# Kernel optimization log

Measured on AMD Instinct MI355X. Metric: run time of the kernel, lower is better.

Reference implementation:

```python
import jax, jax.numpy as jnp
import numpy as np

# ---- static config (mirrors YOLOH_Expand cfg) ----
H, W = 200, 200            # feature map size
A = 9                      # num_anchors
C = 80                     # num_classes
M = H * W * A              # total anchors
K = 1000                   # topk NMS candidates
STRIDE = 16
CTR_CLAMP = 32.0
CONF_THRESH = 0.05
NMS_THRESH = 0.6
SCALE_CLAMP = float(np.log(1000.0 / 16))  # DEFAULT_SCALE_CLAMP
ANCHOR_SIZES = np.array([[32,32],[64,64],[128,128],[32,64],[64,32],
                         [64,128],[128,64],[128,256],[256,128]], dtype=np.float32)


def make_anchors():
    # generate_anchors: meshgrid (+0.5)*stride centers, tiled anchor sizes -> (M,4) cxcywh
    ys, xs = np.meshgrid(np.arange(H), np.arange(W), indexing='ij')
    xy = (np.stack([xs, ys], -1).reshape(-1, 2).astype(np.float32) + 0.5) * STRIDE  # (HW,2)
    xy = np.repeat(xy[:, None, :], A, axis=1)                                       # (HW,A,2)
    wh = np.broadcast_to(ANCHOR_SIZES[None], (H * W, A, 2)).astype(np.float32)
    return jnp.asarray(np.concatenate([xy, wh], -1).reshape(-1, 4))


def setup_inputs() -> dict:
    key = jax.random.key(0)
    k1, k2 = jax.random.split(key)
    return {
        'cls_pred': jax.random.normal(k1, (1, M, C), jnp.float32) - 2.0,  # logits, mostly low conf
        'reg_pred': jax.random.normal(k2, (1, M, 4), jnp.float32) * 0.5,
        'anchor_boxes': make_anchors(),
    }


def decode_boxes(anchors, reg):
    # decode_boxes: clamped center offset + clamped log-scale wh -> x1y1x2y2
    ctr_off = jnp.clip(reg[..., :2] * anchors[..., 2:], -CTR_CLAMP, CTR_CLAMP)
    ctr_xy = anchors[..., :2] + ctr_off
    dwdh = jnp.minimum(reg[..., 2:], SCALE_CLAMP)
    wh = anchors[..., 2:] * jnp.exp(dwdh)
    return jnp.concatenate([ctr_xy - 0.5 * wh, ctr_xy + 0.5 * wh], axis=-1)


def pairwise_iou(b):
    # exact math of YOLOH_Expand.nms
    x1, y1, x2, y2 = b[:, 0], b[:, 1], b[:, 2], b[:, 3]
    areas = (x2 - x1) * (y2 - y1)
    xx1 = jnp.maximum(x1[:, None], x1[None, :])
    yy1 = jnp.maximum(y1[:, None], y1[None, :])
    xx2 = jnp.minimum(x2[:, None], x2[None, :])
    yy2 = jnp.minimum(y2[:, None], y2[None, :])
    w = jnp.maximum(1e-28, xx2 - xx1)
    h = jnp.maximum(1e-28, yy2 - yy1)
    inter = w * h
    return inter / (areas[:, None] + areas[None, :] - inter + 1e-14)


def greedy_nms_keep(iou, cls_ids, valid):
    # per-class greedy NMS over score-sorted candidates: box i is suppressed if
    # any kept higher-score box j of the same class has IoU > thresh.
    same = cls_ids[:, None] == cls_ids[None, :]           # (K,K)
    idx = jnp.arange(K)

    def body(keep, i):
        prior = idx < i
        sup = jnp.any(keep & prior & same[i] & (iou[i] > NMS_THRESH))
        keep = keep.at[i].set((~sup) & valid[i])
        return keep, None

    keep0 = jnp.zeros((K,), dtype=bool)
    keep, _ = jax.lax.scan(body, keep0, idx)
    return keep


def reference(cls_pred, reg_pred, anchor_boxes):
    scores = jax.nn.sigmoid(cls_pred[0])                  # (M,C)
    boxes = decode_boxes(anchor_boxes, reg_pred[0])       # (M,4)
    # postprocess: per-anchor best class + confidence threshold
    cls_inds = jnp.argmax(scores, axis=1)                 # (M,)
    sc = jnp.max(scores, axis=1)                          # (M,)
    valid = sc >= CONF_THRESH
    # fixed-size top-k candidate set (invalid ranked last)
    _, top_i = jax.lax.top_k(jnp.where(valid, sc, -1.0), K)
    b = boxes[top_i]                                      # (K,4)
    s = sc[top_i]                                         # (K,)
    c = cls_inds[top_i]                                   # (K,)
    v = valid[top_i]                                      # (K,)
    iou = pairwise_iou(b)                                 # (K,K)
    keep = greedy_nms_keep(iou, c, v)                     # (K,) bool
    return b, s * keep.astype(s.dtype), c.astype(jnp.int32), keep
```

## Files before the change

kernel.cpp:

```cpp
#include <hip/hip_runtime.h>
#include <math.h>

typedef unsigned long long u64;
typedef unsigned int u32;

#define M_ANCH 360000
#define NCLS 80
#define KTOP 1000
#define CAP 8192
#define NBINS 65536
#define RREP 8
#define CONF_THRESH 0.05f
#define NMS_THRESH 0.6f
#define CTR_CLAMP 32.0f
#define SCALE_CLAMP 4.1351665567423560f

#define AS1 __attribute__((address_space(1)))
#define AS3 __attribute__((address_space(3)))

#define HIST_OFF   0u
#define HIST_BYTES (RREP * NBINS * 4u)
#define CNT_OFF    (HIST_OFF + HIST_BYTES)
#define B_OFF      (CNT_OFF + 4u)
#define VW_OFF     (B_OFF + 4u + 8u)
#define ZERO_END   (VW_OFF + 128u)
#define MERGED_OFF ZERO_END
#define BLKSUM_OFF (MERGED_OFF + NBINS * 4u)
#define CAND_OFF   (BLKSUM_OFF + 256u)
#define SC_OFF     (CAND_OFF + CAP * 8u)
#define CLS_OFF    (SC_OFF + M_ANCH * 4u)
#define SSC_OFF    (CLS_OFF + M_ANCH * 4u)
#define SCLS_OFF   (SSC_OFF + KTOP * 4u)
#define SUP_OFF    ((SCLS_OFF + KTOP * 4u + 15u) & ~15u)

__device__ __forceinline__ u32 fkey(float f) {
    u32 u = __float_as_uint(f);
    return (u & 0x80000000u) ? ~u : (u | 0x80000000u);
}

__global__ __launch_bounds__(256) void k_score(const float* __restrict__ cls_pred,
                                               float* __restrict__ sc_all,
                                               int* __restrict__ cls_all,
                                               u32* __restrict__ hist) {
    __shared__ float4 stage[1280];
    int t = threadIdx.x;
    const float4* gp = (const float4*)cls_pred + (size_t)blockIdx.x * 1280;
#pragma unroll
    for (int k = 0; k < 5; k++) {
        int f = t + 256 * k;
        __builtin_amdgcn_global_load_lds((AS1 void*)(gp + f),
                                         (AS3 void*)(stage + f), 16, 0, 0);
    }
    __syncthreads();

    if (t < 64) {
        const float4* av = stage + t * 20;
        float mv = -1e30f; int mc = 0;
        int k0 = t & 7;
#pragma unroll
        for (int i = 0; i < 20; i++) {
            int k = k0 + i;
            if (k >= 20) k -= 20;
            float4 v = av[k];
            float lm_ = v.x; int lc_ = 4 * k;
            if (v.y > lm_) { lm_ = v.y; lc_ = 4 * k + 1; }
            if (v.z > lm_) { lm_ = v.z; lc_ = 4 * k + 2; }
            if (v.w > lm_) { lm_ = v.w; lc_ = 4 * k + 3; }
            if (lm_ > mv || (lm_ == mv && lc_ < mc)) { mv = lm_; mc = lc_; }
        }
        int a = blockIdx.x * 64 + t;
        float sc = 1.0f / (1.0f + expf(-mv));
        sc_all[a] = sc;
        cls_all[a] = mc;
        float msk = (sc >= CONF_THRESH) ? sc : -1.0f;
        u32 u = fkey(msk);
        atomicAdd(&hist[((blockIdx.x & (RREP - 1)) << 16) + (u >> 16)], 1u);
    }
}

__global__ __launch_bounds__(1024) void k_hsum(const u32* __restrict__ hist,
                                               u32* __restrict__ merged,
                                               u32* __restrict__ blksum) {
    __shared__ u32 red[1024];
    int t = threadIdx.x;
    int b = blockIdx.x * 1024 + t;
    u32 s = 0;
#pragma unroll
    for (int r = 0; r < RREP; r++) s += hist[r * NBINS + b];
    merged[b] = s;
    red[t] = s;
    __syncthreads();
    for (int off = 512; off > 0; off >>= 1) {
        if (t < off) red[t] += red[t + off];
        __syncthreads();
    }
    if (t == 0) blksum[blockIdx.x] = red[0];
}

__global__ __launch_bounds__(1024) void k_boundary(const u32* __restrict__ merged,
                                                   const u32* __restrict__ blksum,
                                                   u32* __restrict__ outB) {
    __shared__ u32 bs[64];
    __shared__ u32 sj, sA;
    __shared__ u32 csum[1024];
    int t = threadIdx.x;
    if (t < 64) bs[t] = blksum[t];
    __syncthreads();
    if (t == 0) {
        u32 cum = 0; u32 j = 0; u32 Aj = 0;
        for (int b = 63; b >= 0; b--) {
            if (cum + bs[b] >= KTOP) { j = (u32)b; Aj = cum; break; }
            cum += bs[b];
        }
        sj = j; sA = Aj;
    }
    __syncthreads();
    u32 j = sj, Aj = sA;
    u32 h = merged[j * 1024 + t];
    csum[t] = h;
    __syncthreads();
    u32 v = h;
    for (int off = 1; off < 1024; off <<= 1) {
        u32 add = (t + off < 1024) ? csum[t + off] : 0u;
        __syncthreads();
        v += add;
        csum[t] = v;
        __syncthreads();
    }
    u32 above = (t == 1023) ? 0u : csum[t + 1];
    if (Aj + above < KTOP && Aj + above + h >= KTOP) outB[0] = j * 1024 + t;
}

__global__ __launch_bounds__(256) void k_compact(const float* __restrict__ sc_all,
                                                 const u32* __restrict__ pB,
                                                 u32* __restrict__ counter,
                                                 u64* __restrict__ cand) {
    int i = blockIdx.x * 256 + threadIdx.x;
    if (i >= M_ANCH) return;
    u32 B = *pB;
    float s = sc_all[i];
    float m = (s >= CONF_THRESH) ? s : -1.0f;
    u32 u = fkey(m);
    if ((u >> 16) >= B) {
        u32 pos = atomicAdd(counter, 1u);
        if (pos < CAP) cand[pos] = ((u64)u << 32) | (u64)(0xFFFFFFFFu - (u32)i);
    }
}

__global__ __launch_bounds__(1024) void k_select(const u64* __restrict__ cand,
                                                 const u32* __restrict__ counter,
                                                 const float* __restrict__ sc_all,
                                                 const int* __restrict__ cls_all,
                                                 const float* __restrict__ reg_pred,
                                                 const float* __restrict__ anchors,
                                                 float* __restrict__ out,
                                                 float* __restrict__ sel_sc,
                                                 int* __restrict__ sel_cls,
                                                 u64* __restrict__ valid_words) {
    __shared__ u64 keys[CAP];
    int t = threadIdx.x;
    u32 n = *counter;
    if (n > CAP) n = CAP;
    u32 P = 1024;
    while (P < n) P <<= 1;
    for (u32 i = t; i < P; i += 1024) keys[i] = (i < n) ? cand[i] : 0ull;
    for (u32 k = 2; k <= P; k <<= 1) {
        for (u32 j = k >> 1; j > 0; j >>= 1) {
            __syncthreads();
            for (u32 i = t; i < P; i += 1024) {
                u32 ixj = i ^ j;
                if (ixj > i) {
                    u64 a = keys[i], b = keys[ixj];
                    bool desc = ((i & k) == 0);
                    if (desc ? (a < b) : (a > b)) { keys[i] = b; keys[ixj] = a; }
                }
            }
        }
    }
    __syncthreads();
    if (t < KTOP) {
        u64 key = keys[t];
        u32 idx = 0xFFFFFFFFu - (u32)(key & 0xFFFFFFFFull);
        if (idx >= M_ANCH) idx = 0;
        float s = sc_all[idx];
        int cl = cls_all[idx];
        float4 a = ((const float4*)anchors)[idx];
        float4 r = ((const float4*)reg_pred)[idx];
        float ox = fminf(fmaxf(r.x * a.z, -CTR_CLAMP), CTR_CLAMP);
        float oy = fminf(fmaxf(r.y * a.w, -CTR_CLAMP), CTR_CLAMP);
        float cx = a.x + ox, cy = a.y + oy;
        float ww = a.z * expf(fminf(r.z, SCALE_CLAMP));
        float hh = a.w * expf(fminf(r.w, SCALE_CLAMP));
        float4 box;
        box.x = cx - 0.5f * ww;
        box.y = cy - 0.5f * hh;
        box.z = cx + 0.5f * ww;
        box.w = cy + 0.5f * hh;
        ((float4*)out)[t] = box;
        out[5 * KTOP + t] = (float)cl;
        sel_sc[t] = s;
        sel_cls[t] = cl;
        if (s >= CONF_THRESH) atomicOr(&valid_words[t >> 6], 1ull << (t & 63));
    }
}

__global__ __launch_bounds__(256) void k_supmat(const float* __restrict__ out,
                                                const int* __restrict__ sel_cls,
                                                u64* __restrict__ sup) {
    int wid = threadIdx.x >> 6;
    int lane = threadIdx.x & 63;
    int g = blockIdx.x * 4 + wid;
    int i = g >> 4;
    int w = g & 15;
    int j = w * 64 + lane;
    int jc = (j < KTOP) ? j : (KTOP - 1);
    float4 bi = ((const float4*)out)[i];
    float4 bj = ((const float4*)out)[jc];
    int ci = sel_cls[i], cj = sel_cls[jc];
    float ai = (bi.z - bi.x) * (bi.w - bi.y);
    float aj = (bj.z - bj.x) * (bj.w - bj.y);
    float xx1 = fmaxf(bi.x, bj.x), yy1 = fmaxf(bi.y, bj.y);
    float xx2 = fminf(bi.z, bj.z), yy2 = fminf(bi.w, bj.w);
    float iw = fmaxf(1e-28f, xx2 - xx1), ih = fmaxf(1e-28f, yy2 - yy1);
    float inter = iw * ih;
    float iou = inter / (ai + aj - inter + 1e-14f);
    bool pred = (j < i) && (ci == cj) && (iou > NMS_THRESH);
    u64 bal = __ballot((int)pred);
    if (lane == 0) sup[g] = bal;
}

__global__ __launch_bounds__(64) void k_nms(const u64* __restrict__ sup,
                                            const u64* __restrict__ valid_words,
                                            const float* __restrict__ sel_sc,
                                            float* __restrict__ out) {
    __shared__ u64 keepA[16];
    int lane = threadIdx.x;
    if (lane < 16) keepA[lane] = 0ull;
    __syncthreads();

    for (int b = 0; b < 16; b++) {
        int row = b * 64 + lane;
        int rowc = (row < KTOP) ? row : (KTOP - 1);
        const ulonglong2* rp = (const ulonglong2*)(sup + (size_t)rowc * 16);
        ulonglong2 q0 = rp[0], q1 = rp[1], q2 = rp[2], q3 = rp[3];
        ulonglong2 q4 = rp[4], q5 = rp[5], q6 = rp[6], q7 = rp[7];
        u64 d = sup[(size_t)rowc * 16 + b];
        u64 vm = valid_words[b];

        u64 acc = (q0.x & keepA[0])  | (q0.y & keepA[1])
                | (q1.x & keepA[2])  | (q1.y & keepA[3])
                | (q2.x & keepA[4])  | (q2.y & keepA[5])
                | (q3.x & keepA[6])  | (q3.y & keepA[7])
                | (q4.x & keepA[8])  | (q4.y & keepA[9])
                | (q5.x & keepA[10]) | (q5.y & keepA[11])
                | (q6.x & keepA[12]) | (q6.y & keepA[13])
                | (q7.x & keepA[14]) | (q7.y & keepA[15]);
        u64 premask = __ballot(acc != 0ull);
        u64 eligible = vm & ~premask;

        u32 dlo = (u32)d, dhi = (u32)(d >> 32);
        u64 kb = 0ull;
#pragma unroll
        for (int j = 0; j < 64; j++) {
            u32 djl = __builtin_amdgcn_readlane(dlo, j);
            u32 djh = __builtin_amdgcn_readlane(dhi, j);
            u64 dj = ((u64)djh << 32) | (u64)djl;
            bool kj = (((eligible >> j) & 1ull) != 0ull) && ((dj & kb) == 0ull);
            kb |= ((u64)(kj ? 1u : 0u)) << j;
        }
        if (lane == 0) keepA[b] = kb;
        __syncthreads();
    }

    for (int t = lane; t < KTOP; t += 64) {
        int kb = (int)((keepA[t >> 6] >> (t & 63)) & 1ull);
        float s = sel_sc[t];
        out[4 * KTOP + t] = kb ? s : 0.0f;
        out[6 * KTOP + t] = (float)kb;
    }
}

extern "C" void kernel_launch(void* const* d_in, const int* in_sizes, int n_in,
                              void* d_out, int out_size, void* d_ws, size_t ws_size,
                              hipStream_t stream) {
    const float* cls_pred = (const float*)d_in[0];
    const float* reg_pred = (const float*)d_in[1];
    const float* anchors  = (const float*)d_in[2];
    float* out = (float*)d_out;
    char* ws = (char*)d_ws;

    u32* hist     = (u32*)(ws + HIST_OFF);
    u32* counter  = (u32*)(ws + CNT_OFF);
    u32* pB       = (u32*)(ws + B_OFF);
    u64* vwords   = (u64*)(ws + VW_OFF);
    u32* merged   = (u32*)(ws + MERGED_OFF);
    u32* blksum   = (u32*)(ws + BLKSUM_OFF);
    u64* cand     = (u64*)(ws + CAND_OFF);
    float* sc_all = (float*)(ws + SC_OFF);
    int* cls_all  = (int*)(ws + CLS_OFF);
    float* sel_sc = (float*)(ws + SSC_OFF);
    int* sel_cls  = (int*)(ws + SCLS_OFF);
    u64* sup      = (u64*)(ws + SUP_OFF);

    hipMemsetAsync(d_ws, 0, ZERO_END, stream);

    int nbs = M_ANCH / 64;
    int nbc = (M_ANCH + 255) / 256;
    k_score<<<nbs, 256, 0, stream>>>(cls_pred, sc_all, cls_all, hist);
    k_hsum<<<NBINS / 1024, 1024, 0, stream>>>(hist, merged, blksum);
    k_boundary<<<1, 1024, 0, stream>>>(merged, blksum, pB);
    k_compact<<<nbc, 256, 0, stream>>>(sc_all, pB, counter, cand);
    k_select<<<1, 1024, 0, stream>>>(cand, counter, sc_all, cls_all, reg_pred,
                                     anchors, out, sel_sc, sel_cls, vwords);
    k_supmat<<<(KTOP * 16) / 4, 256, 0, stream>>>(out, sel_cls, sup);
    k_nms<<<1, 64, 0, stream>>>(sup, vwords, sel_sc, out);
}
```

Measured before the change: 315.3 us.

## Make score kernel persistent with register prefetch and all-thread argmax reduction

The score kernel moves from one block per 64-anchor tile to a fixed grid of 1875 persistent blocks that loop over the tiles. Each thread prefetches the next tile's cls_pred into registers while the current tile is reduced. All 256 threads now do a partial per-float4 argmax, packed as value/class pairs into a double-buffered, padded LDS stage, and finish with lane shuffles. Previously only 64 threads did a serial 20-step scan. Histogram replica selection changes from block index to anchor index, and the direct global-to-LDS loads are dropped in favour of ordinary register loads.

```diff
diff --git a/kernel.cpp b/kernel.cpp
--- a/kernel.cpp
+++ b/kernel.cpp
@@ -15,8 +15,8 @@
 #define CTR_CLAMP 32.0f
 #define SCALE_CLAMP 4.1351665567423560f
 
-#define AS1 __attribute__((address_space(1)))
-#define AS3 __attribute__((address_space(3)))
+#define NTILES 5625
+#define K1_GRID 1875
 
 #define HIST_OFF   0u
 #define HIST_BYTES (RREP * NBINS * 4u)
@@ -38,43 +38,79 @@
     return (u & 0x80000000u) ? ~u : (u | 0x80000000u);
 }
 
+__device__ __forceinline__ u64 pack_mc(float4 v, int cbase) {
+    float m = v.x; int c = cbase;
+    if (v.y > m) { m = v.y; c = cbase + 1; }
+    if (v.z > m) { m = v.z; c = cbase + 2; }
+    if (v.w > m) { m = v.w; c = cbase + 3; }
+    return ((u64)(u32)c << 32) | (u64)__float_as_uint(m);
+}
+
 __global__ __launch_bounds__(256) void k_score(const float* __restrict__ cls_pred,
                                                float* __restrict__ sc_all,
                                                int* __restrict__ cls_all,
                                                u32* __restrict__ hist) {
-    __shared__ float4 stage[1280];
+    __shared__ u64 stage[2][1344];
     int t = threadIdx.x;
-    const float4* gp = (const float4*)cls_pred + (size_t)blockIdx.x * 1280;
+    int a4 = t >> 2, q = t & 3;
+    const float4* base = (const float4*)cls_pred;
+
+    float4 r0, r1, r2, r3, r4;
+    {
+        const float4* gp = base + (size_t)blockIdx.x * 1280;
+        r0 = gp[t];
+        r1 = gp[t + 256];
+        r2 = gp[t + 512];
+        r3 = gp[t + 768];
+        r4 = gp[t + 1024];
+    }
+
+    int p = 0;
+    for (int it = blockIdx.x; it < NTILES; it += K1_GRID) {
+        {
+            int f0 = t, f1 = t + 256, f2 = t + 512, f3 = t + 768, f4 = t + 1024;
+            stage[p][f0 + f0 / 20] = pack_mc(r0, 4 * (f0 % 20));
+            stage[p][f1 + f1 / 20] = pack_mc(r1, 4 * (f1 % 20));
+            stage[p][f2 + f2 / 20] = pack_mc(r2, 4 * (f2 % 20));
+            stage[p][f3 + f3 / 20] = pack_mc(r3, 4 * (f3 % 20));
+            stage[p][f4 + f4 / 20] = pack_mc(r4, 4 * (f4 % 20));
+        }
+        __syncthreads();
+
+        int nt = it + K1_GRID;
+        if (nt < NTILES) {
+            const float4* gp = base + (size_t)nt * 1280;
+            r0 = gp[t];
+            r1 = gp[t + 256];
+            r2 = gp[t + 512];
+            r3 = gp[t + 768];
+            r4 = gp[t + 1024];
+        }
+
+        float mv = -1e30f; int mc = 0;
 #pragma unroll
-    for (int k = 0; k < 5; k++) {
-        int f = t + 256 * k;
-        __builtin_amdgcn_global_load_lds((AS1 void*)(gp + f),
-                                         (AS3 void*)(stage + f), 16, 0, 0);
-    }
-    __syncthreads();
-
-    if (t < 64) {
-        const float4* av = stage + t * 20;
-        float mv = -1e30f; int mc = 0;
-        int k0 = t & 7;
-#pragma unroll
-        for (int i = 0; i < 20; i++) {
-            int k = k0 + i;
-            if (k >= 20) k -= 20;
-            float4 v = av[k];
-            float lm_ = v.x; int lc_ = 4 * k;
-            if (v.y > lm_) { lm_ = v.y; lc_ = 4 * k + 1; }
-            if (v.z > lm_) { lm_ = v.z; lc_ = 4 * k + 2; }
-            if (v.w > lm_) { lm_ = v.w; lc_ = 4 * k + 3; }
-            if (lm_ > mv || (lm_ == mv && lc_ < mc)) { mv = lm_; mc = lc_; }
-        }
-        int a = blockIdx.x * 64 + t;
-        float sc = 1.0f / (1.0f + expf(-mv));
-        sc_all[a] = sc;
-        cls_all[a] = mc;
-        float msk = (sc >= CONF_THRESH) ? sc : -1.0f;
-        u32 u = fkey(msk);
-        atomicAdd(&hist[((blockIdx.x & (RREP - 1)) << 16) + (u >> 16)], 1u);
+        for (int i = 0; i < 5; i++) {
+            u64 w = stage[p][a4 * 21 + q + 4 * i];
+            float v = __uint_as_float((u32)w);
+            int c = (int)(w >> 32);
+            if (v > mv || (v == mv && c < mc)) { mv = v; mc = c; }
+        }
+        {
+            float ov = __shfl_xor(mv, 1); int oc = __shfl_xor(mc, 1);
+            if (ov > mv || (ov == mv && oc < mc)) { mv = ov; mc = oc; }
+            ov = __shfl_xor(mv, 2); oc = __shfl_xor(mc, 2);
+            if (ov > mv || (ov == mv && oc < mc)) { mv = ov; mc = oc; }
+        }
+        if (q == 0) {
+            int a = it * 64 + a4;
+            float sc = 1.0f / (1.0f + expf(-mv));
+            sc_all[a] = sc;
+            cls_all[a] = mc;
+            float msk = (sc >= CONF_THRESH) ? sc : -1.0f;
+            u32 u = fkey(msk);
+            atomicAdd(&hist[((a4 & (RREP - 1)) << 16) + (u >> 16)], 1u);
+        }
+        p ^= 1;
     }
 }
 
@@ -304,9 +340,8 @@
 
     hipMemsetAsync(d_ws, 0, ZERO_END, stream);
 
-    int nbs = M_ANCH / 64;
     int nbc = (M_ANCH + 255) / 256;
-    k_score<<<nbs, 256, 0, stream>>>(cls_pred, sc_all, cls_all, hist);
+    k_score<<<K1_GRID, 256, 0, stream>>>(cls_pred, sc_all, cls_all, hist);
     k_hsum<<<NBINS / 1024, 1024, 0, stream>>>(hist, merged, blksum);
     k_boundary<<<1, 1024, 0, stream>>>(merged, blksum, pB);
     k_compact<<<nbc, 256, 0, stream>>>(sc_all, pB, counter, cand);
```

Result: slower. 411.5 us (+30.5%).
